# Optimization experiments

Hardware: AMD Instinct MI355X
Metric: run time of the kernel (lower is better)

## Reference

```python
import jax, jax.numpy as jnp
import numpy as np
from jax import lax

EPS_IN = 1e-5  # torch InstanceNorm1d eps


def instance_norm(x, w, b):
    # x: (B, C, T); normalize over T per (B, C), biased variance
    mu = x.mean(axis=-1, keepdims=True)
    var = x.var(axis=-1, keepdims=True)
    return (x - mu) * lax.rsqrt(var + EPS_IN) * w[None, :, None] + b[None, :, None]


def conv1x1(x, w):
    # w: (O, I, 1)
    return jnp.einsum('oi,bit->bot', w[:, :, 0], x)


def setup_inputs() -> dict:
    key = jax.random.key(0)
    ks = jax.random.split(key, 16)
    B, C, T, NC = 32, 64, 2048, 4
    enc_dim = C * 3 * 4
    d = {
        'xb': jax.random.normal(ks[0], (B, 3, C, T), jnp.float32),
        'mu': jnp.linspace(-3.0, 3.0, 4),
        'sigma': jnp.full((4,), 2.0),
        'sconv1_w': jax.random.normal(ks[1], (128, enc_dim, 1)) * (1.0 / np.sqrt(enc_dim)),
        'in1_w': 1.0 + 0.1 * jax.random.normal(ks[2], (128,)),
        'in1_b': 0.1 * jax.random.normal(ks[3], (128,)),
        'sconv2_w': jax.random.normal(ks[4], (C, 128, 1)) * (1.0 / np.sqrt(128)),
        'in2_w': 1.0 + 0.1 * jax.random.normal(ks[5], (C,)),
        'in2_b': 0.1 * jax.random.normal(ks[6], (C,)),
        'tconv1_w': jax.random.normal(ks[7], (C, C, 15)) * (1.0 / np.sqrt(C * 15)),
        'in3_w': 1.0 + 0.1 * jax.random.normal(ks[8], (C,)),
        'in3_b': 0.1 * jax.random.normal(ks[9], (C,)),
        'tconv2_w': jax.random.normal(ks[10], (C, C, 1)) * (1.0 / np.sqrt(C)),
        'in4_w': 1.0 + 0.1 * jax.random.normal(ks[11], (C,)),
        'in4_b': 0.1 * jax.random.normal(ks[12], (C,)),
        'alpha': jnp.asarray(0.5),
        'gamma': jnp.asarray(0.5),
        'beta_logit': jnp.asarray(1.0),
        'fc_w': jax.random.normal(ks[13], (4, C)) * (1.0 / np.sqrt(C)),
        'fc_b': 0.1 * jax.random.normal(ks[14], (4,)),
    }
    return d


def reference(xb, mu, sigma, sconv1_w, in1_w, in1_b, sconv2_w, in2_w, in2_b,
              tconv1_w, in3_w, in3_b, tconv2_w, in4_w, in4_b,
              alpha, gamma, beta_logit, fc_w, fc_b):
    B, Ftypes, C, T = xb.shape
    V_BASE = 1.0
    Tp = T // 8

    # pooled curvature / tangent streams -> (T', B, C)
    curv_p = xb[:, 1].reshape(B, C, Tp, 8).mean(-1).transpose(2, 0, 1)
    tang_p = xb[:, 2].reshape(B, C, Tp, 8).mean(-1).transpose(2, 0, 1)

    # learnable population encoding: (B,3,C,T,4) -> (B, 3*C*4, T)
    enc = jnp.exp(-(xb[..., None] - mu) ** 2 / (2.0 * sigma ** 2 + 1e-6))
    x_enc = enc.transpose(0, 1, 2, 4, 3).reshape(B, Ftypes * C * 4, T)

    # spatial 1x1 convs + instance norm + relu
    h = jax.nn.relu(instance_norm(conv1x1(x_enc, sconv1_w), in1_w, in1_b))
    h = jax.nn.relu(instance_norm(conv1x1(h, sconv2_w), in2_w, in2_b))

    # temporal conv k=15 pad=7, 1x1 conv, avg pool 8
    h = lax.conv_general_dilated(h, tconv1_w, (1,), [(7, 7)],
                                 dimension_numbers=('NCH', 'OIH', 'NCH'))
    h = jax.nn.relu(instance_norm(h, in3_w, in3_b))
    h = jax.nn.relu(instance_norm(conv1x1(h, tconv2_w), in4_w, in4_b))
    h = h.reshape(B, C, Tp, 8).mean(-1)  # AvgPool1d(8)
    # dropout is identity in eval mode
    c = h.transpose(2, 0, 1)  # (T', B, C)

    # sequential GD-LIF recurrence over T' steps
    def step(m, inp):
        x_t, curv_t, tang_t = inp
        v_th = V_BASE + alpha * tang_t
        beta = jax.nn.sigmoid(beta_logit - gamma * curv_t)
        m_next = beta * m + x_t
        spike = (m_next - v_th > 0).astype(m_next.dtype)
        m_next = m_next - spike * v_th
        return m_next, spike

    m0 = jnp.zeros((B, C), xb.dtype)
    _, spikes = lax.scan(step, m0, (c, curv_p, tang_p))  # (T', B, C)

    attn = jax.nn.softmax(curv_p, axis=0)
    out_feat = jnp.sum(spikes * attn, axis=0)  # (B, C)
    return out_feat @ fc_w.T + fc_b
```

## Files before the change

### kernel.cpp

```cpp
#include <hip/hip_runtime.h>
#include <math.h>

#define TLEN 2048
#define TP 256

typedef double d4 __attribute__((ext_vector_type(4)));

__device__ __forceinline__ double block_reduce_sum_d(double v, double* sm) {
#pragma unroll
  for (int off = 32; off > 0; off >>= 1) v += __shfl_down(v, off, 64);
  int lane = threadIdx.x & 63, wid = threadIdx.x >> 6;
  __syncthreads();
  if (lane == 0) sm[wid] = v;
  __syncthreads();
  double r = sm[0] + sm[1] + sm[2] + sm[3];
  __syncthreads();
  return r;
}

__global__ void k_probe_f64(int* __restrict__ tbl) {
  int l = threadIdx.x;
  __shared__ int kaS[64], kbS[64];
  __shared__ int cnt[256];
  int rdv[4] = {-1, -1, -1, -1}, cdv[4] = {-1, -1, -1, -1};
  int mav = -1, nbv = -1;
  int okr = 1;
  int nrow = 0, ncol = 0;
  kaS[l] = -1; kbS[l] = -1;
  __syncthreads();

  for (int j = 0; j < 64; ++j) {
    double a = (l == j) ? 1.0 : 0.0;
    d4 acc = {0.0, 0.0, 0.0, 0.0};
    acc = __builtin_amdgcn_mfma_f64_16x16x4f64(a, 1.0, acc, 0, 0, 0);
    int mylab = -1;
#pragma unroll
    for (int v = 0; v < 4; ++v) if (acc[v] != 0.0 && rdv[v] >= 0) mylab = rdv[v];
#pragma unroll
    for (int off = 32; off >= 1; off >>= 1) {
      int o = __shfl_xor(mylab, off);
      mylab = mylab > o ? mylab : o;
    }
    int label = (mylab < 0) ? nrow : mylab;
    if (mylab < 0) nrow++;
    if (label >= 16) okr = 0;
#pragma unroll
    for (int v = 0; v < 4; ++v) if (acc[v] != 0.0) rdv[v] = label;
    if (l == j) mav = label;
  }

  for (int j = 0; j < 64; ++j) {
    double bb = (l == j) ? 1.0 : 0.0;
    d4 acc = {0.0, 0.0, 0.0, 0.0};
    acc = __builtin_amdgcn_mfma_f64_16x16x4f64(1.0, bb, acc, 0, 0, 0);
    int mylab = -1;
#pragma unroll
    for (int v = 0; v < 4; ++v) if (acc[v] != 0.0 && cdv[v] >= 0) mylab = cdv[v];
#pragma unroll
    for (int off = 32; off >= 1; off >>= 1) {
      int o = __shfl_xor(mylab, off);
      mylab = mylab > o ? mylab : o;
    }
    int label = (mylab < 0) ? ncol : mylab;
    if (mylab < 0) ncol++;
    if (label >= 16) okr = 0;
#pragma unroll
    for (int v = 0; v < 4; ++v) if (acc[v] != 0.0) cdv[v] = label;
    if (l == j) nbv = label;
  }

  unsigned long long row0 = __ballot(mav == 0);
  if (__popcll(row0) != 4) okr = 0;
  for (int i = 0; i < 4; ++i) {
    int rep = -1, idx = -1;
    for (int t = 0; t < 64; ++t)
      if ((row0 >> t) & 1ull) { if (++idx == i) { rep = t; break; } }
    double a = (l == rep) ? 1.0 : 0.0;
    double bb = (double)(l + 1);
    d4 acc = {0.0, 0.0, 0.0, 0.0};
    acc = __builtin_amdgcn_mfma_f64_16x16x4f64(a, bb, acc, 0, 0, 0);
#pragma unroll
    for (int v = 0; v < 4; ++v)
      if (rdv[v] == 0) {
        int jp = (int)(acc[v] + 0.5) - 1;
        if (jp >= 0 && jp < 64) kbS[jp] = i; else okr = 0;
      }
  }
  __syncthreads();
  int kbv = kbS[l];

  for (int i = 0; i < 4; ++i) {
    unsigned long long bm = __ballot(kbv == i);
    int rep = -1;
    if (bm != 0ull) { rep = 0; while (!((bm >> rep) & 1ull)) ++rep; }
    else okr = 0;
    int nc = (rep >= 0) ? __shfl(nbv, rep) : -2;
    double bb = (l == rep) ? 1.0 : 0.0;
    double aa = (double)(l + 1);
    d4 acc = {0.0, 0.0, 0.0, 0.0};
    acc = __builtin_amdgcn_mfma_f64_16x16x4f64(aa, bb, acc, 0, 0, 0);
#pragma unroll
    for (int v = 0; v < 4; ++v)
      if (cdv[v] == nc) {
        int jp = (int)(acc[v] + 0.5) - 1;
        if (jp >= 0 && jp < 64) kaS[jp] = i; else okr = 0;
      }
  }
  __syncthreads();
  int kav = kaS[l];

  if (nrow != 16 || ncol != 16) okr = 0;
  if (mav < 0 || mav > 15 || nbv < 0 || nbv > 15 ||
      kav < 0 || kav > 3 || kbv < 0 || kbv > 3) okr = 0;
#pragma unroll
  for (int v = 0; v < 4; ++v)
    if (rdv[v] < 0 || rdv[v] > 15 || cdv[v] < 0 || cdv[v] > 15) okr = 0;
  cnt[l] = 0; cnt[64 + l] = 0; cnt[128 + l] = 0; cnt[192 + l] = 0;
  __syncthreads();
  if (mav >= 0 && mav < 16 && kav >= 0 && kav < 4) atomicAdd(&cnt[mav * 4 + kav], 1);
  if (kbv >= 0 && kbv < 4 && nbv >= 0 && nbv < 16) atomicAdd(&cnt[64 + kbv * 16 + nbv], 1);
  __syncthreads();
  if (cnt[l] != 1 || cnt[64 + l] != 1) okr = 0;
  __syncthreads();
  cnt[l] = 0; cnt[64 + l] = 0; cnt[128 + l] = 0; cnt[192 + l] = 0;
  __syncthreads();
#pragma unroll
  for (int v = 0; v < 4; ++v)
    if (rdv[v] >= 0 && rdv[v] < 16 && cdv[v] >= 0 && cdv[v] < 16)
      atomicAdd(&cnt[rdv[v] * 16 + cdv[v]], 1);
  __syncthreads();
#pragma unroll
  for (int v = 0; v < 4; ++v) if (cnt[l * 4 + v] != 1) okr = 0;
  if (mav == 0) {
    int rank = (int)__popcll(row0 & ((1ull << l) - 1ull));
    if (kav != rank) okr = 0;
  }
  unsigned long long good = __ballot(okr != 0);
  tbl[l] = mav; tbl[64 + l] = kav; tbl[128 + l] = kbv; tbl[192 + l] = nbv;
#pragma unroll
  for (int v = 0; v < 4; ++v) {
    tbl[256 + l * 4 + v] = rdv[v];
    tbl[512 + l * 4 + v] = cdv[v];
  }
  if (l == 0) tbl[768] = (good == 0xFFFFFFFFFFFFFFFFull) ? 1 : 0;
}

__global__ void k_repack_w(const float* __restrict__ w, float* __restrict__ wT) {
  int idx = blockIdx.x * 256 + threadIdx.x;
  if (idx >= 64 * 64 * 15) return;
  int o = idx & 63, i = (idx >> 6) & 63, k = idx >> 12;
  wT[idx] = w[(o * 64 + i) * 15 + k];
}

template <typename T>
__global__ __launch_bounds__(256) void k_pool_ct(const float* __restrict__ xb,
                                                 T* __restrict__ curvp,
                                                 T* __restrict__ tangp) {
  int row = blockIdx.x;
  int b = row >> 6, c = row & 63;
  int tid = threadIdx.x;
  const float* s1 = xb + ((size_t)((b * 3 + 1) * 64 + c)) * TLEN + tid * 8;
  const float* s2 = xb + ((size_t)((b * 3 + 2) * 64 + c)) * TLEN + tid * 8;
  double p1 = 0.0, p2 = 0.0;
#pragma unroll
  for (int j = 0; j < 8; ++j) { p1 += (double)s1[j]; p2 += (double)s2[j]; }
  curvp[(size_t)row * TP + tid] = (T)(p1 * 0.125);
  tangp[(size_t)row * TP + tid] = (T)(p2 * 0.125);
}

template <typename T>
__global__ __launch_bounds__(256, 4) void k_enc1_mfma(const float* __restrict__ xb,
                                                      const float* __restrict__ w,
                                                      const float* __restrict__ mu,
                                                      const float* __restrict__ sigma,
                                                      T* __restrict__ h1,
                                                      const int* __restrict__ tbl) {
  if (tbl[768] == 0) return;
  __shared__ float AsT[32][132];
  __shared__ double Bs[32][68];
  __shared__ double smu[4], sinv[4];
  int b = blockIdx.x, t0 = blockIdx.y * 64, tid = threadIdx.x;
  int wv = tid >> 6, l = tid & 63;
  int t_ma = tbl[l], t_ka = tbl[64 + l], t_kb = tbl[128 + l], t_nb = tbl[192 + l];
  int t_rd[4], t_cd[4];
#pragma unroll
  for (int v = 0; v < 4; ++v) { t_rd[v] = tbl[256 + l * 4 + v]; t_cd[v] = tbl[512 + l * 4 + v]; }
  if (tid < 4) {
    smu[tid] = (double)mu[tid];
    double s = (double)sigma[tid];
    sinv[tid] = 1.0 / (2.0 * s * s + 1e-6);
  }
  d4 acc[2][4];
#pragma unroll
  for (int r = 0; r < 2; ++r)
#pragma unroll
    for (int c = 0; c < 4; ++c) acc[r][c] = (d4){0.0, 0.0, 0.0, 0.0};

  for (int kc = 0; kc < 24; ++kc) {
    int i0 = kc * 32;
    __syncthreads();
    {
      int idx = tid * 4;
#pragma unroll
      for (int rep = 0; rep < 4; ++rep) {
        int o = idx >> 5, ii = idx & 31;
        float4 v4 = *(const float4*)(w + (size_t)o * 768 + i0 + ii);
        AsT[ii][o] = v4.x; AsT[ii + 1][o] = v4.y; AsT[ii + 2][o] = v4.z; AsT[ii + 3][o] = v4.w;
        idx += 1024;
      }
    }
    {
      int f = i0 >> 8;
      int cb = (i0 >> 2) & 63;
      int c = tid >> 5, l2 = tid & 31;
      int t = 2 * l2;
      float2 x2 = *(const float2*)(xb + ((size_t)((b * 3 + f) * 64 + cb + c)) * TLEN + t0 + t);
      double xv0 = (double)x2.x, xv1 = (double)x2.y;
#pragma unroll
      for (int g = 0; g < 4; ++g) {
        double m = smu[g], inv = sinv[g];
        double d0 = xv0 - m, d1 = xv1 - m;
        double2 e = {exp(-d0 * d0 * inv), exp(-d1 * d1 * inv)};
        *(double2*)&Bs[c * 4 + g][t] = e;
      }
    }
    __syncthreads();
#pragma unroll
    for (int k4 = 0; k4 < 32; k4 += 4) {
      double aF0 = (double)AsT[k4 + t_ka][wv * 32 + t_ma];
      double aF1 = (double)AsT[k4 + t_ka][wv * 32 + 16 + t_ma];
      double bF[4];
#pragma unroll
      for (int c = 0; c < 4; ++c) bF[c] = Bs[k4 + t_kb][c * 16 + t_nb];
#pragma unroll
      for (int c = 0; c < 4; ++c) {
        acc[0][c] = __builtin_amdgcn_mfma_f64_16x16x4f64(aF0, bF[c], acc[0][c], 0, 0, 0);
        acc[1][c] = __builtin_amdgcn_mfma_f64_16x16x4f64(aF1, bF[c], acc[1][c], 0, 0, 0);
      }
    }
  }
#pragma unroll
  for (int r = 0; r < 2; ++r)
#pragma unroll
    for (int c = 0; c < 4; ++c)
#pragma unroll
      for (int v = 0; v < 4; ++v) {
        int o = wv * 32 + r * 16 + t_rd[v];
        h1[((size_t)(b * 128 + o)) * TLEN + t0 + c * 16 + t_cd[v]] = (T)acc[r][c][v];
      }
}

template <typename T>
__global__ __launch_bounds__(256, 4) void k_enc1_valu(const float* __restrict__ xb,
                                                      const float* __restrict__ w,
                                                      const float* __restrict__ mu,
                                                      const float* __restrict__ sigma,
                                                      T* __restrict__ h1,
                                                      const int* __restrict__ tbl) {
  if (tbl[768] != 0) return;
  __shared__ float AsT[32][132];
  __shared__ double Bs[32][64];
  __shared__ double smu[4], sinv[4];
  int b = blockIdx.x, t0 = blockIdx.y * 64, tid = threadIdx.x;
  if (tid < 4) {
    smu[tid] = (double)mu[tid];
    double s = (double)sigma[tid];
    sinv[tid] = 1.0 / (2.0 * s * s + 1e-6);
  }
  double acc[8][4] = {};
  int to = (tid >> 4) * 8, l = tid & 15;
  for (int kc = 0; kc < 24; ++kc) {
    int i0 = kc * 32;
    __syncthreads();
    {
      int idx = tid * 4;
#pragma unroll
      for (int rep = 0; rep < 4; ++rep) {
        int o = idx >> 5, ii = idx & 31;
        float4 v4 = *(const float4*)(w + (size_t)o * 768 + i0 + ii);
        AsT[ii][o] = v4.x; AsT[ii + 1][o] = v4.y; AsT[ii + 2][o] = v4.z; AsT[ii + 3][o] = v4.w;
        idx += 1024;
      }
    }
    {
      int f = i0 >> 8;
      int cb = (i0 >> 2) & 63;
      int c = tid >> 5, l2 = tid & 31;
      int t = 2 * l2;
      float2 x2 = *(const float2*)(xb + ((size_t)((b * 3 + f) * 64 + cb + c)) * TLEN + t0 + t);
      double xv0 = (double)x2.x, xv1 = (double)x2.y;
#pragma unroll
      for (int g = 0; g < 4; ++g) {
        double m = smu[g], inv = sinv[g];
        double d0 = xv0 - m, d1 = xv1 - m;
        double2 e = {exp(-d0 * d0 * inv), exp(-d1 * d1 * inv)};
        *(double2*)&Bs[c * 4 + g][t] = e;
      }
    }
    __syncthreads();
#pragma unroll
    for (int kk = 0; kk < 32; ++kk) {
      float4 a0 = *(const float4*)&AsT[kk][to];
      float4 a1 = *(const float4*)&AsT[kk][to + 4];
      double a[8] = {(double)a0.x, (double)a0.y, (double)a0.z, (double)a0.w,
                     (double)a1.x, (double)a1.y, (double)a1.z, (double)a1.w};
      double bb[4];
#pragma unroll
      for (int j = 0; j < 2; ++j) {
        double2 p = *(const double2*)&Bs[kk][2 * l + 32 * j];
        bb[2 * j] = p.x; bb[2 * j + 1] = p.y;
      }
#pragma unroll
      for (int q = 0; q < 8; ++q)
#pragma unroll
        for (int j = 0; j < 4; ++j) acc[q][j] += a[q] * bb[j];
    }
  }
#pragma unroll
  for (int q = 0; q < 8; ++q) {
    T* op = h1 + ((size_t)(b * 128 + to + q)) * TLEN + t0;
    op[2 * l]      = (T)acc[q][0];
    op[2 * l + 1]  = (T)acc[q][1];
    op[2 * l + 32] = (T)acc[q][2];
    op[2 * l + 33] = (T)acc[q][3];
  }
}

template <int K, typename T>
__global__ __launch_bounds__(256, 4) void k_conv1x1_mfma(const T* __restrict__ in,
                                                         const float* __restrict__ w,
                                                         T* __restrict__ out,
                                                         const int* __restrict__ tbl) {
  if (tbl[768] == 0) return;
  __shared__ float AsT[32][68];
  __shared__ double Bs[32][68];
  int b = blockIdx.x, t0 = blockIdx.y * 64, tid = threadIdx.x;
  int wv = tid >> 6, l = tid & 63;
  int t_ma = tbl[l], t_ka = tbl[64 + l], t_kb = tbl[128 + l], t_nb = tbl[192 + l];
  int t_rd[4], t_cd[4];
#pragma unroll
  for (int v = 0; v < 4; ++v) { t_rd[v] = tbl[256 + l * 4 + v]; t_cd[v] = tbl[512 + l * 4 + v]; }
  int o0 = wv * 16;
  d4 acc[4];
#pragma unroll
  for (int c = 0; c < 4; ++c) acc[c] = (d4){0.0, 0.0, 0.0, 0.0};
  for (int kc = 0; kc < K / 32; ++kc) {
    __syncthreads();
    {
      int idx = tid * 4;
#pragma unroll
      for (int rep = 0; rep < 2; ++rep) {
        int o = idx >> 5, ii = idx & 31;
        float4 v4 = *(const float4*)(w + (size_t)o * K + kc * 32 + ii);
        AsT[ii][o] = v4.x; AsT[ii + 1][o] = v4.y; AsT[ii + 2][o] = v4.z; AsT[ii + 3][o] = v4.w;
        idx += 1024;
      }
    }
    {
      int r = tid >> 3, l8 = tid & 7;
      const T* gp = in + ((size_t)(b * K + kc * 32 + r)) * TLEN + t0;
#pragma unroll
      for (int q = 0; q < 4; ++q) {
        int t = 2 * l8 + 16 * q;
        double2 v = {(double)gp[t], (double)gp[t + 1]};
        *(double2*)&Bs[r][t] = v;
      }
    }
    __syncthreads();
#pragma unroll
    for (int k4 = 0; k4 < 32; k4 += 4) {
      double aF = (double)AsT[k4 + t_ka][o0 + t_ma];
#pragma unroll
      for (int c = 0; c < 4; ++c) {
        double bF = Bs[k4 + t_kb][c * 16 + t_nb];
        acc[c] = __builtin_amdgcn_mfma_f64_16x16x4f64(aF, bF, acc[c], 0, 0, 0);
      }
    }
  }
#pragma unroll
  for (int c = 0; c < 4; ++c)
#pragma unroll
    for (int v = 0; v < 4; ++v)
      out[((size_t)(b * 64 + o0 + t_rd[v])) * TLEN + t0 + c * 16 + t_cd[v]] = (T)acc[c][v];
}

template <int K, typename T>
__global__ __launch_bounds__(256, 4) void k_conv1x1_valu(const T* __restrict__ in,
                                                         const float* __restrict__ w,
                                                         T* __restrict__ out,
                                                         const int* __restrict__ tbl) {
  if (tbl[768] != 0) return;
  __shared__ float AsT[32][68];
  __shared__ double Bs[32][64];
  int b = blockIdx.x, t0 = blockIdx.y * 64, tid = threadIdx.x;
  double acc[4][4] = {};
  int to = (tid >> 4) * 4, l = tid & 15;
  for (int kc = 0; kc < K / 32; ++kc) {
    __syncthreads();
    {
      int idx = tid * 4;
#pragma unroll
      for (int rep = 0; rep < 2; ++rep) {
        int o = idx >> 5, ii = idx & 31;
        float4 v4 = *(const float4*)(w + (size_t)o * K + kc * 32 + ii);
        AsT[ii][o] = v4.x; AsT[ii + 1][o] = v4.y; AsT[ii + 2][o] = v4.z; AsT[ii + 3][o] = v4.w;
        idx += 1024;
      }
    }
    {
      int r = tid >> 3, l8 = tid & 7;
      const T* gp = in + ((size_t)(b * K + kc * 32 + r)) * TLEN + t0;
#pragma unroll
      for (int q = 0; q < 4; ++q) {
        int t = 2 * l8 + 16 * q;
        double2 v = {(double)gp[t], (double)gp[t + 1]};
        *(double2*)&Bs[r][t] = v;
      }
    }
    __syncthreads();
#pragma unroll
    for (int kk = 0; kk < 32; ++kk) {
      float4 a4 = *(const float4*)&AsT[kk][to];
      double a0 = (double)a4.x, a1 = (double)a4.y, a2 = (double)a4.z, a3 = (double)a4.w;
      double bb[4];
#pragma unroll
      for (int j = 0; j < 2; ++j) {
        double2 p = *(const double2*)&Bs[kk][2 * l + 32 * j];
        bb[2 * j] = p.x; bb[2 * j + 1] = p.y;
      }
#pragma unroll
      for (int j = 0; j < 4; ++j) {
        acc[0][j] += a0 * bb[j];
        acc[1][j] += a1 * bb[j];
        acc[2][j] += a2 * bb[j];
        acc[3][j] += a3 * bb[j];
      }
    }
  }
#pragma unroll
  for (int q = 0; q < 4; ++q) {
    T* op = out + ((size_t)(b * 64 + to + q)) * TLEN + t0;
    op[2 * l]      = (T)acc[q][0];
    op[2 * l + 1]  = (T)acc[q][1];
    op[2 * l + 32] = (T)acc[q][2];
    op[2 * l + 33] = (T)acc[q][3];
  }
}

template <typename T>
__global__ __launch_bounds__(256) void k_tconv1(const T* __restrict__ h2,
                                                const float* __restrict__ wT,
                                                T* __restrict__ h3) {
  __shared__ __align__(16) double In[64][80];
  __shared__ float Ws[8][15][64];
  int b = blockIdx.x, t0 = blockIdx.y * 64, tid = threadIdx.x;
  for (int idx = tid; idx < 64 * 78; idx += 256) {
    int i = idx / 78, x = idx - i * 78;
    int tg = t0 - 7 + x;
    double v = 0.0;
    if (tg >= 0 && tg < TLEN) v = (double)h2[((size_t)(b * 64 + i)) * TLEN + tg];
    In[i][x] = v;
  }
  double acc[4][4] = {};
  int og = (tid >> 4) * 4, tt2 = (tid & 15) * 4;
  for (int ic = 0; ic < 8; ++ic) {
    __syncthreads();
    for (int idx = tid; idx < 15 * 8 * 16; idx += 256) {
      int k = idx >> 7;
      int r = idx & 127;
      int ii = r >> 4, o4 = (r & 15) * 4;
      float4 v = *(const float4*)(wT + ((size_t)(k * 64 + ic * 8 + ii)) * 64 + o4);
      *(float4*)&Ws[ii][k][o4] = v;
    }
    __syncthreads();
#pragma unroll
    for (int ii = 0; ii < 8; ++ii) {
      int i = ic * 8 + ii;
      double r[18];
#pragma unroll
      for (int m = 0; m < 18; m += 2) {
        double2 p = *(const double2*)&In[i][tt2 + m];
        r[m] = p.x; r[m + 1] = p.y;
      }
#pragma unroll
      for (int k = 0; k < 15; ++k) {
        float4 w4 = *(const float4*)&Ws[ii][k][og];
        double w0 = (double)w4.x, w1 = (double)w4.y, w2 = (double)w4.z, w3 = (double)w4.w;
#pragma unroll
        for (int j = 0; j < 4; ++j) {
          double x = r[j + k];
          acc[0][j] += w0 * x;
          acc[1][j] += w1 * x;
          acc[2][j] += w2 * x;
          acc[3][j] += w3 * x;
        }
      }
    }
  }
#pragma unroll
  for (int q = 0; q < 4; ++q) {
    T* op = h3 + ((size_t)(b * 64 + og + q)) * TLEN + t0 + tt2;
#pragma unroll
    for (int j = 0; j < 4; ++j) op[j] = (T)acc[q][j];
  }
}

template <typename T>
__global__ __launch_bounds__(256) void k_instnorm_relu(T* __restrict__ h,
                                                       const float* __restrict__ gw,
                                                       const float* __restrict__ gb,
                                                       int chmask) {
  __shared__ double sm[4];
  int row = blockIdx.x, tid = threadIdx.x;
  int ch = row & chmask;
  T* base = h + (size_t)row * TLEN + tid * 8;
  double v[8];
#pragma unroll
  for (int j = 0; j < 8; ++j) v[j] = (double)base[j];
  double s = 0.0;
#pragma unroll
  for (int j = 0; j < 8; ++j) s += v[j];
  double mean = block_reduce_sum_d(s, sm) * (1.0 / 2048.0);
  double sq = 0.0;
#pragma unroll
  for (int j = 0; j < 8; ++j) { double d = v[j] - mean; sq += d * d; }
  double var = block_reduce_sum_d(sq, sm) * (1.0 / 2048.0);
  double scale = (double)gw[ch] / sqrt(var + 1e-5);
  double shift = (double)gb[ch] - mean * scale;
#pragma unroll
  for (int j = 0; j < 8; ++j) base[j] = (T)fmax(v[j] * scale + shift, 0.0);
}

template <typename T>
__global__ __launch_bounds__(256) void k_in4_pool(const T* __restrict__ h,
                                                  const float* __restrict__ gw,
                                                  const float* __restrict__ gb,
                                                  T* __restrict__ cbuf) {
  __shared__ double sm[4];
  int row = blockIdx.x, tid = threadIdx.x;
  int ch = row & 63;
  const T* base = h + (size_t)row * TLEN + tid * 8;
  double v[8];
#pragma unroll
  for (int j = 0; j < 8; ++j) v[j] = (double)base[j];
  double s = 0.0;
#pragma unroll
  for (int j = 0; j < 8; ++j) s += v[j];
  double mean = block_reduce_sum_d(s, sm) * (1.0 / 2048.0);
  double sq = 0.0;
#pragma unroll
  for (int j = 0; j < 8; ++j) { double d = v[j] - mean; sq += d * d; }
  double var = block_reduce_sum_d(sq, sm) * (1.0 / 2048.0);
  double scale = (double)gw[ch] / sqrt(var + 1e-5);
  double shift = (double)gb[ch] - mean * scale;
  double p = 0.0;
#pragma unroll
  for (int j = 0; j < 8; ++j) p += fmax(v[j] * scale + shift, 0.0);
  cbuf[(size_t)row * TP + tid] = (T)(p * 0.125);
}

template <typename T>
__global__ __launch_bounds__(64) void k_scan(const T* __restrict__ cbuf,
                                             const T* __restrict__ curvp,
                                             const T* __restrict__ tangp,
                                             const float* __restrict__ alpha,
                                             const float* __restrict__ gamma,
                                             const float* __restrict__ betal,
                                             double* __restrict__ ofeat) {
  int id = blockIdx.x * 64 + threadIdx.x;
  double a = (double)alpha[0], g = (double)gamma[0], bl = (double)betal[0];
  const T* cu_p = curvp + (size_t)id * TP;
  const T* ta_p = tangp + (size_t)id * TP;
  const T* cb_p = cbuf + (size_t)id * TP;
  double mmax = -1e300, ssum = 0.0;
  for (int tp = 0; tp < TP; ++tp) {
    double v = (double)cu_p[tp];
    double nm = fmax(mmax, v);
    ssum = ssum * exp(mmax - nm) + exp(v - nm);
    mmax = nm;
  }
  double invs = 1.0 / ssum;
  double mem = 0.0, acc = 0.0;
  for (int tp = 0; tp < TP; ++tp) {
    double x = (double)cb_p[tp];
    double cu = (double)cu_p[tp];
    double ta = (double)ta_p[tp];
    double vth = 1.0 + a * ta;
    double beta = 1.0 / (1.0 + exp(g * cu - bl));
    mem = beta * mem + x;
    if (mem - vth > 0.0) {
      acc += exp(cu - mmax) * invs;
      mem -= vth;
    }
  }
  ofeat[id] = acc;
}

__global__ void k_fc(const double* __restrict__ ofeat, const float* __restrict__ fw,
                     const float* __restrict__ fb, float* __restrict__ out) {
  int tid = threadIdx.x;
  if (tid >= 128) return;
  int b = tid >> 2, j = tid & 3;
  double s = (double)fb[j];
#pragma unroll
  for (int c = 0; c < 64; ++c) s += ofeat[b * 64 + c] * (double)fw[j * 64 + c];
  out[b * 4 + j] = (float)s;
}

template <typename T>
static void run_all(void* const* d_in, float* out, char* wsb, hipStream_t stream) {
  const float* xb    = (const float*)d_in[0];
  const float* mu    = (const float*)d_in[1];
  const float* sigma = (const float*)d_in[2];
  const float* w1    = (const float*)d_in[3];
  const float* in1w  = (const float*)d_in[4];
  const float* in1b  = (const float*)d_in[5];
  const float* w2    = (const float*)d_in[6];
  const float* in2w  = (const float*)d_in[7];
  const float* in2b  = (const float*)d_in[8];
  const float* wt1   = (const float*)d_in[9];
  const float* in3w  = (const float*)d_in[10];
  const float* in3b  = (const float*)d_in[11];
  const float* w4    = (const float*)d_in[12];
  const float* in4w  = (const float*)d_in[13];
  const float* in4b  = (const float*)d_in[14];
  const float* alpha = (const float*)d_in[15];
  const float* gamma = (const float*)d_in[16];
  const float* betal = (const float*)d_in[17];
  const float* fcw   = (const float*)d_in[18];
  const float* fcb   = (const float*)d_in[19];

  size_t sT = sizeof(T);
  T* h1 = (T*)wsb;
  T* h2 = (T*)(wsb + (size_t)8388608 * sT);
  T* h3 = h1;
  T* h4 = h2;
  float* wT = (float*)(wsb + (size_t)12582912 * sT);
  char* p = wsb + (size_t)12582912 * sT + 245760;
  T* curvp = (T*)p;
  T* tangp = (T*)(p + (size_t)524288 * sT);
  T* cbuf  = (T*)(p + (size_t)2 * 524288 * sT);
  double* ofeat = (double*)(p + (size_t)3 * 524288 * sT);
  int* tbl = (int*)cbuf;

  k_repack_w<<<dim3(240), dim3(256), 0, stream>>>(wt1, wT);
  k_pool_ct<T><<<dim3(2048), dim3(256), 0, stream>>>(xb, curvp, tangp);
  k_probe_f64<<<dim3(1), dim3(64), 0, stream>>>(tbl);
  k_enc1_mfma<T><<<dim3(32, 32), dim3(256), 0, stream>>>(xb, w1, mu, sigma, h1, tbl);
  k_enc1_valu<T><<<dim3(32, 32), dim3(256), 0, stream>>>(xb, w1, mu, sigma, h1, tbl);
  k_instnorm_relu<T><<<dim3(4096), dim3(256), 0, stream>>>(h1, in1w, in1b, 127);
  k_conv1x1_mfma<128, T><<<dim3(32, 32), dim3(256), 0, stream>>>(h1, w2, h2, tbl);
  k_conv1x1_valu<128, T><<<dim3(32, 32), dim3(256), 0, stream>>>(h1, w2, h2, tbl);
  k_instnorm_relu<T><<<dim3(2048), dim3(256), 0, stream>>>(h2, in2w, in2b, 63);
  k_tconv1<T><<<dim3(32, 32), dim3(256), 0, stream>>>(h2, wT, h3);
  k_instnorm_relu<T><<<dim3(2048), dim3(256), 0, stream>>>(h3, in3w, in3b, 63);
  k_conv1x1_mfma<64, T><<<dim3(32, 32), dim3(256), 0, stream>>>(h3, w4, h4, tbl);
  k_conv1x1_valu<64, T><<<dim3(32, 32), dim3(256), 0, stream>>>(h3, w4, h4, tbl);
  k_in4_pool<T><<<dim3(2048), dim3(256), 0, stream>>>(h4, in4w, in4b, cbuf);
  k_scan<T><<<dim3(32), dim3(64), 0, stream>>>(cbuf, curvp, tangp, alpha, gamma, betal, ofeat);
  k_fc<<<dim3(1), dim3(128), 0, stream>>>(ofeat, fcw, fcb, out);
}

extern "C" void kernel_launch(void* const* d_in, const int* in_sizes, int n_in,
                              void* d_out, int out_size, void* d_ws, size_t ws_size,
                              hipStream_t stream) {
  const size_t NEED64 = 113508352ull;
  if (ws_size >= NEED64)
    run_all<double>(d_in, (float*)d_out, (char*)d_ws, stream);
  else
    run_all<float>(d_in, (float*)d_out, (char*)d_ws, stream);
}
```

Baseline: 711.4 us.

## Fuse instance-norm apply into consumer convs and add MFMA path for temporal conv

Splits instance norm into a stats-only kernel that writes per-row scale/shift, and applies the normalization and ReLU while loading inputs in the following conv kernels, removing the full read-modify-write pass over each activation tensor. Also adds an f64 MFMA version of the k=15 temporal conv, gated by the probe table like the other MFMA kernels. The conv loaders now do extra FMA work per element, and the scale/shift arrays share the cbuf scratch region with the probe table.

```diff
diff --git a/kernel.cpp b/kernel.cpp
--- a/kernel.cpp
+++ b/kernel.cpp
@@ -166,6 +166,33 @@
   for (int j = 0; j < 8; ++j) { p1 += (double)s1[j]; p2 += (double)s2[j]; }
   curvp[(size_t)row * TP + tid] = (T)(p1 * 0.125);
   tangp[(size_t)row * TP + tid] = (T)(p2 * 0.125);
+}
+
+template <typename T>
+__global__ __launch_bounds__(256) void k_stats(const T* __restrict__ h,
+                                               const float* __restrict__ gw,
+                                               const float* __restrict__ gb,
+                                               int chmask,
+                                               double* __restrict__ sc,
+                                               double* __restrict__ sh) {
+  __shared__ double sm[4];
+  int row = blockIdx.x, tid = threadIdx.x;
+  int ch = row & chmask;
+  const T* base = h + (size_t)row * TLEN + tid * 8;
+  double v[8];
+#pragma unroll
+  for (int j = 0; j < 8; ++j) v[j] = (double)base[j];
+  double s = 0.0;
+#pragma unroll
+  for (int j = 0; j < 8; ++j) s += v[j];
+  double mean = block_reduce_sum_d(s, sm) * (1.0 / 2048.0);
+  double sq = 0.0;
+#pragma unroll
+  for (int j = 0; j < 8; ++j) { double d = v[j] - mean; sq += d * d; }
+  double var = block_reduce_sum_d(sq, sm) * (1.0 / 2048.0);
+  double scale = (double)gw[ch] / sqrt(var + 1e-5);
+  double shift = (double)gb[ch] - mean * scale;
+  if (tid == 0) { sc[row] = scale; sh[row] = shift; }
 }
 
 template <typename T>
@@ -329,6 +356,8 @@
 template <int K, typename T>
 __global__ __launch_bounds__(256, 4) void k_conv1x1_mfma(const T* __restrict__ in,
                                                          const float* __restrict__ w,
+                                                         const double* __restrict__ sc,
+                                                         const double* __restrict__ sh,
                                                          T* __restrict__ out,
                                                          const int* __restrict__ tbl) {
   if (tbl[768] == 0) return;
@@ -358,11 +387,14 @@
     }
     {
       int r = tid >> 3, l8 = tid & 7;
-      const T* gp = in + ((size_t)(b * K + kc * 32 + r)) * TLEN + t0;
+      int srow = b * K + kc * 32 + r;
+      const T* gp = in + (size_t)srow * TLEN + t0;
+      double s_ = sc[srow], h_ = sh[srow];
 #pragma unroll
       for (int q = 0; q < 4; ++q) {
         int t = 2 * l8 + 16 * q;
-        double2 v = {(double)gp[t], (double)gp[t + 1]};
+        double2 v = {fmax((double)gp[t] * s_ + h_, 0.0),
+                     fmax((double)gp[t + 1] * s_ + h_, 0.0)};
         *(double2*)&Bs[r][t] = v;
       }
     }
@@ -387,6 +419,8 @@
 template <int K, typename T>
 __global__ __launch_bounds__(256, 4) void k_conv1x1_valu(const T* __restrict__ in,
                                                          const float* __restrict__ w,
+                                                         const double* __restrict__ sc,
+                                                         const double* __restrict__ sh,
                                                          T* __restrict__ out,
                                                          const int* __restrict__ tbl) {
   if (tbl[768] != 0) return;
@@ -409,11 +443,14 @@
     }
     {
       int r = tid >> 3, l8 = tid & 7;
-      const T* gp = in + ((size_t)(b * K + kc * 32 + r)) * TLEN + t0;
+      int srow = b * K + kc * 32 + r;
+      const T* gp = in + (size_t)srow * TLEN + t0;
+      double s_ = sc[srow], h_ = sh[srow];
 #pragma unroll
       for (int q = 0; q < 4; ++q) {
         int t = 2 * l8 + 16 * q;
-        double2 v = {(double)gp[t], (double)gp[t + 1]};
+        double2 v = {fmax((double)gp[t] * s_ + h_, 0.0),
+                     fmax((double)gp[t + 1] * s_ + h_, 0.0)};
         *(double2*)&Bs[r][t] = v;
       }
     }
@@ -448,17 +485,82 @@
 }
 
 template <typename T>
-__global__ __launch_bounds__(256) void k_tconv1(const T* __restrict__ h2,
-                                                const float* __restrict__ wT,
-                                                T* __restrict__ h3) {
+__global__ __launch_bounds__(256, 2) void k_tconv1_mfma(const T* __restrict__ h2,
+                                                        const float* __restrict__ wT,
+                                                        const double* __restrict__ sc,
+                                                        const double* __restrict__ sh,
+                                                        T* __restrict__ h3,
+                                                        const int* __restrict__ tbl) {
+  if (tbl[768] == 0) return;
+  __shared__ __align__(16) double In[64][80];
+  __shared__ float Ws[8][15][64];
+  int b = blockIdx.x, t0 = blockIdx.y * 64, tid = threadIdx.x;
+  int wv = tid >> 6, l = tid & 63;
+  int t_ma = tbl[l], t_ka = tbl[64 + l], t_kb = tbl[128 + l], t_nb = tbl[192 + l];
+  int t_rd[4], t_cd[4];
+#pragma unroll
+  for (int v = 0; v < 4; ++v) { t_rd[v] = tbl[256 + l * 4 + v]; t_cd[v] = tbl[512 + l * 4 + v]; }
+  int o0 = wv * 16;
+  for (int idx = tid; idx < 64 * 78; idx += 256) {
+    int i = idx / 78, x = idx - i * 78;
+    int tg = t0 - 7 + x;
+    int row = b * 64 + i;
+    double v = 0.0;
+    if (tg >= 0 && tg < TLEN)
+      v = fmax((double)h2[(size_t)row * TLEN + tg] * sc[row] + sh[row], 0.0);
+    In[i][x] = v;
+  }
+  d4 acc[4];
+#pragma unroll
+  for (int c = 0; c < 4; ++c) acc[c] = (d4){0.0, 0.0, 0.0, 0.0};
+  for (int ic = 0; ic < 8; ++ic) {
+    __syncthreads();
+    for (int idx = tid; idx < 15 * 8 * 16; idx += 256) {
+      int k = idx >> 7;
+      int r = idx & 127;
+      int ii = r >> 4, o4 = (r & 15) * 4;
+      float4 v = *(const float4*)(wT + ((size_t)(k * 64 + ic * 8 + ii)) * 64 + o4);
+      *(float4*)&Ws[ii][k][o4] = v;
+    }
+    __syncthreads();
+#pragma unroll
+    for (int k = 0; k < 15; ++k) {
+#pragma unroll
+      for (int kg = 0; kg < 2; ++kg) {
+        double aF = (double)Ws[kg * 4 + t_ka][k][o0 + t_ma];
+#pragma unroll
+        for (int c = 0; c < 4; ++c) {
+          double bF = In[ic * 8 + kg * 4 + t_kb][c * 16 + t_nb + k];
+          acc[c] = __builtin_amdgcn_mfma_f64_16x16x4f64(aF, bF, acc[c], 0, 0, 0);
+        }
+      }
+    }
+  }
+#pragma unroll
+  for (int c = 0; c < 4; ++c)
+#pragma unroll
+    for (int v = 0; v < 4; ++v)
+      h3[((size_t)(b * 64 + o0 + t_rd[v])) * TLEN + t0 + c * 16 + t_cd[v]] = (T)acc[c][v];
+}
+
+template <typename T>
+__global__ __launch_bounds__(256) void k_tconv1_valu(const T* __restrict__ h2,
+                                                     const float* __restrict__ wT,
+                                                     const double* __restrict__ sc,
+                                                     const double* __restrict__ sh,
+                                                     T* __restrict__ h3,
+                                                     const int* __restrict__ tbl) {
+  if (tbl[768] != 0) return;
   __shared__ __align__(16) double In[64][80];
   __shared__ float Ws[8][15][64];
   int b = blockIdx.x, t0 = blockIdx.y * 64, tid = threadIdx.x;
   for (int idx = tid; idx < 64 * 78; idx += 256) {
     int i = idx / 78, x = idx - i * 78;
     int tg = t0 - 7 + x;
+    int row = b * 64 + i;
     double v = 0.0;
-    if (tg >= 0 && tg < TLEN) v = (double)h2[((size_t)(b * 64 + i)) * TLEN + tg];
+    if (tg >= 0 && tg < TLEN)
+      v = fmax((double)h2[(size_t)row * TLEN + tg] * sc[row] + sh[row], 0.0);
     In[i][x] = v;
   }
   double acc[4][4] = {};
@@ -503,32 +605,6 @@
 #pragma unroll
     for (int j = 0; j < 4; ++j) op[j] = (T)acc[q][j];
   }
-}
-
-template <typename T>
-__global__ __launch_bounds__(256) void k_instnorm_relu(T* __restrict__ h,
-                                                       const float* __restrict__ gw,
-                                                       const float* __restrict__ gb,
-                                                       int chmask) {
-  __shared__ double sm[4];
-  int row = blockIdx.x, tid = threadIdx.x;
-  int ch = row & chmask;
-  T* base = h + (size_t)row * TLEN + tid * 8;
-  double v[8];
-#pragma unroll
-  for (int j = 0; j < 8; ++j) v[j] = (double)base[j];
-  double s = 0.0;
-#pragma unroll
-  for (int j = 0; j < 8; ++j) s += v[j];
-  double mean = block_reduce_sum_d(s, sm) * (1.0 / 2048.0);
-  double sq = 0.0;
-#pragma unroll
-  for (int j = 0; j < 8; ++j) { double d = v[j] - mean; sq += d * d; }
-  double var = block_reduce_sum_d(sq, sm) * (1.0 / 2048.0);
-  double scale = (double)gw[ch] / sqrt(var + 1e-5);
-  double shift = (double)gb[ch] - mean * scale;
-#pragma unroll
-  for (int j = 0; j < 8; ++j) base[j] = (T)fmax(v[j] * scale + shift, 0.0);
 }
 
 template <typename T>
@@ -641,21 +717,29 @@
   T* tangp = (T*)(p + (size_t)524288 * sT);
   T* cbuf  = (T*)(p + (size_t)2 * 524288 * sT);
   double* ofeat = (double*)(p + (size_t)3 * 524288 * sT);
-  int* tbl = (int*)cbuf;
+  char* cb = (char*)cbuf;
+  int* tbl = (int*)cb;
+  double* sc1 = (double*)(cb + 16384);
+  double* sh1 = sc1 + 4096;
+  double* sc2 = sh1 + 4096;
+  double* sh2 = sc2 + 2048;
+  double* sc3 = sh2 + 2048;
+  double* sh3 = sc3 + 2048;
 
   k_repack_w<<<dim3(240), dim3(256), 0, stream>>>(wt1, wT);
   k_pool_ct<T><<<dim3(2048), dim3(256), 0, stream>>>(xb, curvp, tangp);
   k_probe_f64<<<dim3(1), dim3(64), 0, stream>>>(tbl);
   k_enc1_mfma<T><<<dim3(32, 32), dim3(256), 0, stream>>>(xb, w1, mu, sigma, h1, tbl);
   k_enc1_valu<T><<<dim3(32, 32), dim3(256), 0, stream>>>(xb, w1, mu, sigma, h1, tbl);
-  k_instnorm_relu<T><<<dim3(4096), dim3(256), 0, stream>>>(h1, in1w, in1b, 127);
-  k_conv1x1_mfma<128, T><<<dim3(32, 32), dim3(256), 0, stream>>>(h1, w2, h2, tbl);
-  k_conv1x1_valu<128, T><<<dim3(32, 32), dim3(256), 0, stream>>>(h1, w2, h2, tbl);
-  k_instnorm_relu<T><<<dim3(2048), dim3(256), 0, stream>>>(h2, in2w, in2b, 63);
-  k_tconv1<T><<<dim3(32, 32), dim3(256), 0, stream>>>(h2, wT, h3);
-  k_instnorm_relu<T><<<dim3(2048), dim3(256), 0, stream>>>(h3, in3w, in3b, 63);
-  k_conv1x1_mfma<64, T><<<dim3(32, 32), dim3(256), 0, stream>>>(h3, w4, h4, tbl);
-  k_conv1x1_valu<64, T><<<dim3(32, 32), dim3(256), 0, stream>>>(h3, w4, h4, tbl);
+  k_stats<T><<<dim3(4096), dim3(256), 0, stream>>>(h1, in1w, in1b, 127, sc1, sh1);
+  k_conv1x1_mfma<128, T><<<dim3(32, 32), dim3(256), 0, stream>>>(h1, w2, sc1, sh1, h2, tbl);
+  k_conv1x1_valu<128, T><<<dim3(32, 32), dim3(256), 0, stream>>>(h1, w2, sc1, sh1, h2, tbl);
+  k_stats<T><<<dim3(2048), dim3(256), 0, stream>>>(h2, in2w, in2b, 63, sc2, sh2);
+  k_tconv1_mfma<T><<<dim3(32, 32), dim3(256), 0, stream>>>(h2, wT, sc2, sh2, h3, tbl);
+  k_tconv1_valu<T><<<dim3(32, 32), dim3(256), 0, stream>>>(h2, wT, sc2, sh2, h3, tbl);
+  k_stats<T><<<dim3(2048), dim3(256), 0, stream>>>(h3, in3w, in3b, 63, sc3, sh3);
+  k_conv1x1_mfma<64, T><<<dim3(32, 32), dim3(256), 0, stream>>>(h3, w4, sc3, sh3, h4, tbl);
+  k_conv1x1_valu<64, T><<<dim3(32, 32), dim3(256), 0, stream>>>(h3, w4, sc3, sh3, h4, tbl);
   k_in4_pool<T><<<dim3(2048), dim3(256), 0, stream>>>(h4, in4w, in4b, cbuf);
   k_scan<T><<<dim3(32), dim3(64), 0, stream>>>(cbuf, curvp, tangp, alpha, gamma, betal, ofeat);
   k_fc<<<dim3(1), dim3(128), 0, stream>>>(ofeat, fcw, fcb, out);
```

After: 641.4 us. 9.8% less time.
